# Performance work log

Measured on AMD Instinct MI355X. Metric: run time of the kernel, lower is better.

## Reference

```python
import jax, jax.numpy as jnp
import numpy as np

B, C, H, W = 8, 3, 256, 256
K = 32          # num_kernels
P = 7           # patch_size (hard-coded in CUTSEncoder)
HALF = P // 2
NUM_PATCHES = 32
BN_EPS = 1e-5


def _conv_bn_lrelu(x, w, b, gamma, beta):
    # Conv2d(kernel=3, padding='same') + BatchNorm2d (training-mode batch stats) + leaky_relu(0.01)
    y = jax.lax.conv_general_dilated(x, w, window_strides=(1, 1), padding='SAME',
                                     dimension_numbers=('NCHW', 'OIHW', 'NCHW'))
    y = y + b[None, :, None, None]
    m = jnp.mean(y, axis=(0, 2, 3), keepdims=True)
    v = jnp.var(y, axis=(0, 2, 3), keepdims=True)
    y = (y - m) * jax.lax.rsqrt(v + BN_EPS)
    y = gamma[None, :, None, None] * y + beta[None, :, None, None]
    return jax.nn.leaky_relu(y, negative_slope=0.01)


def setup_inputs() -> dict:
    key = jax.random.key(0)
    ks = jax.random.split(key, 16)
    image = jax.random.normal(ks[0], (B, C, H, W), dtype=jnp.float32)
    # coordinates in [HALF, H - P + HALF] so every centered 7x7 slice is in-bounds
    def xy(k):
        return jax.random.randint(k, (B, NUM_PATCHES, 2), HALF, H - P + HALF + 1, dtype=jnp.int32)
    anchors_xy = xy(ks[1])
    positives_xy = xy(ks[2])
    negatives_xy = xy(ks[3])
    conv1_w = jax.random.normal(ks[4], (K, C, 3, 3), jnp.float32) * 0.1
    conv1_b = jnp.zeros((K,), jnp.float32)
    conv2_w = jax.random.normal(ks[5], (2 * K, K, 3, 3), jnp.float32) * 0.06
    conv2_b = jnp.zeros((2 * K,), jnp.float32)
    conv3_w = jax.random.normal(ks[6], (4 * K, 2 * K, 3, 3), jnp.float32) * 0.04
    conv3_b = jnp.zeros((4 * K,), jnp.float32)
    bn1_g, bn1_b = jnp.ones((K,), jnp.float32), jnp.zeros((K,), jnp.float32)
    bn2_g, bn2_b = jnp.ones((2 * K,), jnp.float32), jnp.zeros((2 * K,), jnp.float32)
    bn3_g, bn3_b = jnp.ones((4 * K,), jnp.float32), jnp.zeros((4 * K,), jnp.float32)
    recon_w = jax.random.normal(ks[7], (C * P * P, 4 * K), jnp.float32) * 0.05
    recon_b = jnp.zeros((C * P * P,), jnp.float32)
    return dict(image=image, anchors_xy=anchors_xy, positives_xy=positives_xy,
                negatives_xy=negatives_xy, conv1_w=conv1_w, conv1_b=conv1_b,
                bn1_g=bn1_g, bn1_b=bn1_b, conv2_w=conv2_w, conv2_b=conv2_b,
                bn2_g=bn2_g, bn2_b=bn2_b, conv3_w=conv3_w, conv3_b=conv3_b,
                bn3_g=bn3_g, bn3_b=bn3_b, recon_w=recon_w, recon_b=recon_b)


def reference(image, anchors_xy, positives_xy, negatives_xy,
              conv1_w, conv1_b, bn1_g, bn1_b,
              conv2_w, conv2_b, bn2_g, bn2_b,
              conv3_w, conv3_b, bn3_g, bn3_b,
              recon_w, recon_b):
    z = _conv_bn_lrelu(image, conv1_w, conv1_b, bn1_g, bn1_b)
    z = _conv_bn_lrelu(z, conv2_w, conv2_b, bn2_g, bn2_b)
    z = _conv_bn_lrelu(z, conv3_w, conv3_b, bn3_g, bn3_b)   # [B, 4K, H, W]

    # In the source, the inner patch loop overwrites the buffers every iteration,
    # so only the LAST patch index survives. Gather exactly that, vectorized over batch.
    a_xy = anchors_xy[:, -1, :]
    p_xy = positives_xy[:, -1, :]
    n_xy = negatives_xy[:, -1, :]

    def slice_patch(img, xy):  # img: [C,H,W], xy: [2]
        return jax.lax.dynamic_slice(img, (0, xy[0] - HALF, xy[1] - HALF), (C, P, P))

    anchor_patches = jax.vmap(slice_patch)(image, a_xy)     # [B, C, P, P]
    positive_patches = jax.vmap(slice_patch)(image, p_xy)
    negative_patches = jax.vmap(slice_patch)(image, n_xy)

    def gather_feat(zb, xy):  # zb: [4K,H,W]
        return jax.lax.dynamic_slice(zb, (0, xy[0], xy[1]), (4 * K, 1, 1)).reshape(4 * K)

    # NOTE: source indexes z at negatives_xy (faithfully replicated)
    encoded_anchor_patches = jax.vmap(gather_feat)(z, n_xy)  # [B, 4K]

    # x_recon is computed in the source but not returned; keep the compute for faithfulness
    _x_recon = encoded_anchor_patches @ recon_w.T + recon_b

    return (anchor_patches, positive_patches, negative_patches, encoded_anchor_patches)
```

## Files before the change

kernel.cpp:

```cpp
#include <hip/hip_runtime.h>
#include <math.h>

#define HH 256
#define WW 256
#define BATCH 8
#define HWSZ 65536
#define NPB2 4096

typedef __attribute__((ext_vector_type(8))) short short8;
typedef __attribute__((ext_vector_type(4))) float floatx4;

__device__ __forceinline__ unsigned short f2bf(float f) {
  union { float f; unsigned int u; } v; v.f = f;
  return (unsigned short)((v.u + 0x8000u) >> 16);
}
__device__ __forceinline__ unsigned int pack2bf(float a, float d) {
  union { float f; unsigned int u; } va, vd; va.f = a; vd.f = d;
  return ((va.u + 0x8000u) >> 16) | ((vd.u + 0x8000u) & 0xffff0000u);
}
__device__ __forceinline__ float bf2f(unsigned short u) {
  union { unsigned int u; float f; } v; v.u = ((unsigned int)u) << 16;
  return v.f;
}

__global__ __launch_bounds__(256) void conv1_mfma(
    const float* __restrict__ img, const float* __restrict__ w1,
    const float* __restrict__ bias, unsigned short* __restrict__ out,
    float* __restrict__ partial,
    const float* __restrict__ w2, const float* __restrict__ w3,
    unsigned short* __restrict__ wf2, unsigned short* __restrict__ wf3)
{
  const int lin = blockIdx.x;
  if (lin >= 4096) {
    int idx = (lin - 4096) * 256 + threadIdx.x;
    if (idx < 18432) {
      const int j = idx & 7;
      const int lane = (idx >> 3) & 63;
      int rest = idx >> 9;
      const int ng = rest % 4;
      const int tap = rest / 4;
      const int cout = ng * 16 + (lane & 15);
      const int cin = ((lane >> 4) << 3) + j;
      wf2[idx] = f2bf(w2[((size_t)cout * 32 + cin) * 9 + tap]);
    } else {
      idx -= 18432;
      if (idx >= 73728) return;
      const int j = idx & 7;
      const int lane = (idx >> 3) & 63;
      int rest = idx >> 9;
      const int ng = rest % 8; rest /= 8;
      const int kc = rest & 1;
      const int tap = rest >> 1;
      const int cout = ng * 16 + (lane & 15);
      const int cin = kc * 32 + ((lane >> 4) << 3) + j;
      wf3[idx] = f2bf(w3[((size_t)cout * 64 + cin) * 9 + tap]);
    }
    return;
  }

  const int tid = threadIdx.x, lane = tid & 63, wv = tid >> 6;
  const int wave_m = wv >> 1, wave_n = wv & 1;
  const int xcd = lin & 7, slot = lin >> 3;
  const int b = slot >> 6;
  const int rem = slot & 63;
  const int h0 = ((xcd << 4) + (rem >> 2)) * 2;
  const int w0 = (rem & 3) * 64;

  __shared__ __align__(16) unsigned short simg[4 * 66 * 4];
  __shared__ __align__(16) unsigned short swf[2 * 64 * 8];
  __shared__ float red2[2][4][16];

  for (int t = tid; t < (4 * 66 * 4) / 2; t += 256)
    ((unsigned int*)simg)[t] = 0u;
  {
    const int t0 = tid * 4;
    #pragma unroll
    for (int u = 0; u < 4; ++u) {
      const int idx = t0 + u;
      const int j = idx & 7, l8 = (idx >> 3) & 63, nt = idx >> 9;
      const int k = ((l8 >> 4) << 3) + j;
      const int cout = nt * 16 + (l8 & 15);
      swf[idx] = (k < 27) ? f2bf(w1[cout * 27 + k]) : (unsigned short)0;
    }
  }
  __syncthreads();
  for (int t = tid; t < 792; t += 256) {
    const int ci = t / 264, r2 = t - ci * 264;
    const int r = r2 / 66, px = r2 - r * 66;
    const int hi = h0 + r - 1, wi = w0 + px - 1;
    if ((unsigned)hi < 256u && (unsigned)wi < 256u)
      simg[(r * 66 + px) * 4 + ci] =
          f2bf(img[((size_t)(b * 3 + ci) * 256 + hi) * 256 + wi]);
  }
  __syncthreads();

  const int j15 = lane & 15, q4 = lane >> 4;
  int off[8];
  #pragma unroll
  for (int j = 0; j < 8; ++j) {
    const int k = q4 * 8 + j;
    const int ci = k / 9, tap = k - ci * 9;
    const int dh = tap / 3, dw = tap - dh * 3;
    off[j] = (dh * 66 + dw) * 4 + ci;
  }
  const int base_px = wave_m * 32 + j15;
  const short8 bg = *(const short8*)&swf[(wave_n * 64 + lane) * 8];

  floatx4 acc[2][2];
  #pragma unroll
  for (int rr = 0; rr < 2; ++rr)
    #pragma unroll
    for (int mf = 0; mf < 2; ++mf) {
      acc[rr][mf] = (floatx4){0.f, 0.f, 0.f, 0.f};
      union { short8 v; unsigned short e[8]; } a;
      const int ab = (rr * 66 + base_px + mf * 16) * 4;
      #pragma unroll
      for (int j = 0; j < 8; ++j) a.e[j] = simg[ab + off[j]];
      acc[rr][mf] = __builtin_amdgcn_mfma_f32_16x16x32_bf16(a.v, bg, acc[rr][mf], 0, 0, 0);
    }

  float sa = 0.f, qa = 0.f;
  const float bv = bias[wave_n * 16 + j15];
  #pragma unroll
  for (int rr = 0; rr < 2; ++rr) {
    const size_t orow = ((size_t)(b * 256 + (h0 + rr)) * 256 + w0);
    #pragma unroll
    for (int mf = 0; mf < 2; ++mf)
      #pragma unroll
      for (int r4 = 0; r4 < 4; ++r4) {
        float y = acc[rr][mf][r4] + bv;
        sa += y; qa += y * y;
        const int p = wave_m * 32 + mf * 16 + q4 * 4 + r4;
        out[(orow + p) * 32 + wave_n * 16 + j15] = f2bf(y);
      }
  }
  sa += __shfl_xor(sa, 16); sa += __shfl_xor(sa, 32);
  qa += __shfl_xor(qa, 16); qa += __shfl_xor(qa, 32);
  if (lane < 16) { red2[0][wv][lane] = sa; red2[1][wv][lane] = qa; }
  __syncthreads();
  if (tid < 64) {
    const int c = tid >> 1, jj = tid & 1;
    const int wn = c >> 4, li = c & 15;
    const float r = red2[jj][wn][li] + red2[jj][wn + 2][li];
    partial[((size_t)c * 2 + jj) * NPB2 + lin] = r;
  }
}

template<int CIN, int COUT, bool WRITE_OUT, int MINW>
__global__ __launch_bounds__(256, MINW) void conv_mfma(
    const unsigned short* __restrict__ in, const unsigned short* __restrict__ wf,
    const float* __restrict__ bias,
    const float* __restrict__ bn_sc, const float* __restrict__ bn_sh,
    unsigned short* __restrict__ out, float* __restrict__ partial)
{
  constexpr int KC = CIN / 32;
  constexpr int NG = COUT / 16;
  constexpr int NF = COUT / 32;
  constexpr int CH8 = CIN / 8;
  constexpr int CH8_LOG = (CH8 == 4) ? 2 : 3;
  constexpr int CPAD = CIN + 8;
  constexpr int CHUNKS = 4 * 66 * CH8;

  const int tid = threadIdx.x, lane = tid & 63, wv = tid >> 6;
  const int wave_m = wv >> 1, wave_n = wv & 1;

  const int lin = blockIdx.x;
  const int xcd = lin & 7, slot = lin >> 3;
  const int b = slot >> 6;
  const int rem = slot & 63;
  const int h0 = ((xcd << 4) + (rem >> 2)) * 2;
  const int w0 = (rem & 3) * 64;
  const size_t inb = (size_t)b * HWSZ * CIN;

  __shared__ __align__(16) unsigned short lds[4 * 66 * CPAD];

  for (int c = tid; c < CHUNKS; c += 256) {
    const int r = c / (66 * CH8);
    const int rem2 = c - r * (66 * CH8);
    const int px = rem2 >> CH8_LOG, ck = rem2 & (CH8 - 1);
    const int hi = h0 + r - 1, wi = w0 - 1 + px;
    uint4 v = make_uint4(0u, 0u, 0u, 0u);
    if ((unsigned)hi < 256u && (unsigned)wi < 256u) {
      uint4 raw = *(const uint4*)&in[inb + ((size_t)hi * 256 + wi) * CIN + ck * 8];
      const float4 s0 = *(const float4*)&bn_sc[ck * 8];
      const float4 s1 = *(const float4*)&bn_sc[ck * 8 + 4];
      const float4 t0 = *(const float4*)&bn_sh[ck * 8];
      const float4 t1 = *(const float4*)&bn_sh[ck * 8 + 4];
      const float scs[8] = {s0.x, s0.y, s0.z, s0.w, s1.x, s1.y, s1.z, s1.w};
      const float shs[8] = {t0.x, t0.y, t0.z, t0.w, t1.x, t1.y, t1.z, t1.w};
      unsigned int* u = (unsigned int*)&raw;
      unsigned int* o = (unsigned int*)&v;
      #pragma unroll
      for (int p = 0; p < 4; ++p) {
        float a = bf2f((unsigned short)(u[p] & 0xffff));
        float d = bf2f((unsigned short)(u[p] >> 16));
        float ya = a * scs[2 * p] + shs[2 * p];
        float yd = d * scs[2 * p + 1] + shs[2 * p + 1];
        ya = fmaxf(ya, 0.01f * ya);
        yd = fmaxf(yd, 0.01f * yd);
        o[p] = pack2bf(ya, yd);
      }
    }
    *(uint4*)&lds[(r * 66 + px) * CPAD + ck * 8] = v;
  }
  __syncthreads();

  const int j15 = lane & 15, q4 = lane >> 4;
  const int base_px = wave_m * 32 + j15;
  const unsigned short* abase = &lds[base_px * CPAD + q4 * 8];

  floatx4 acc[2][2][NF];
  #pragma unroll
  for (int rr = 0; rr < 2; ++rr)
    #pragma unroll
    for (int mf = 0; mf < 2; ++mf)
      #pragma unroll
      for (int nf = 0; nf < NF; ++nf) acc[rr][mf][nf] = (floatx4){0.f, 0.f, 0.f, 0.f};

  #pragma unroll
  for (int dh = 0; dh < 3; ++dh) {
    #pragma unroll
    for (int dw = 0; dw < 3; ++dw) {
      #pragma unroll
      for (int kc = 0; kc < KC; ++kc) {
        const int tap = dh * 3 + dw;
        short8 bg[NF];
        #pragma unroll
        for (int nf = 0; nf < NF; ++nf)
          bg[nf] = *(const short8*)&wf[((((tap * KC + kc) * NG) + wave_n * NF + nf) * 64 + lane) * 8];
        #pragma unroll
        for (int rr = 0; rr < 2; ++rr) {
          short8 a[2];
          #pragma unroll
          for (int mf = 0; mf < 2; ++mf)
            a[mf] = *(const short8*)&abase[((rr + dh) * 66 + dw + mf * 16) * CPAD + kc * 32];
          #pragma unroll
          for (int mf = 0; mf < 2; ++mf)
            #pragma unroll
            for (int nf = 0; nf < NF; ++nf)
              acc[rr][mf][nf] = __builtin_amdgcn_mfma_f32_16x16x32_bf16(a[mf], bg[nf], acc[rr][mf][nf], 0, 0, 0);
        }
      }
    }
  }

  float bv[NF], sa[NF], qa[NF];
  #pragma unroll
  for (int nf = 0; nf < NF; ++nf) {
    bv[nf] = bias[wave_n * (COUT / 2) + nf * 16 + j15];
    sa[nf] = 0.f; qa[nf] = 0.f;
  }
  #pragma unroll
  for (int rr = 0; rr < 2; ++rr) {
    const size_t orow = ((size_t)(b * 256 + (h0 + rr)) * 256 + w0);
    #pragma unroll
    for (int nf = 0; nf < NF; ++nf) {
      const int ch = wave_n * (COUT / 2) + nf * 16 + j15;
      #pragma unroll
      for (int mf = 0; mf < 2; ++mf)
        #pragma unroll
        for (int r4 = 0; r4 < 4; ++r4) {
          float y = acc[rr][mf][nf][r4] + bv[nf];
          sa[nf] += y; qa[nf] += y * y;
          if constexpr (WRITE_OUT) {
            const int p = wave_m * 32 + mf * 16 + q4 * 4 + r4;
            out[(orow + p) * COUT + ch] = f2bf(y);
          }
        }
    }
  }

  __syncthreads();
  float* red = (float*)lds;
  #pragma unroll
  for (int nf = 0; nf < NF; ++nf) {
    float s = sa[nf], q = qa[nf];
    s += __shfl_xor(s, 16); s += __shfl_xor(s, 32);
    q += __shfl_xor(q, 16); q += __shfl_xor(q, 32);
    if (lane < 16) {
      red[(wv * NF + nf) * 16 + lane] = s;
      red[4 * NF * 16 + (wv * NF + nf) * 16 + lane] = q;
    }
  }
  __syncthreads();
  if (tid < COUT) {
    const int wn = tid / (COUT / 2), rr = tid % (COUT / 2);
    const int nf = rr >> 4, li = rr & 15;
    float s = red[(wn * NF + nf) * 16 + li] + red[((wn + 2) * NF + nf) * 16 + li];
    float q = red[4 * NF * 16 + (wn * NF + nf) * 16 + li] +
              red[4 * NF * 16 + ((wn + 2) * NF + nf) * 16 + li];
    partial[((size_t)tid * 2 + 0) * NPB2 + lin] = s;
    partial[((size_t)tid * 2 + 1) * NPB2 + lin] = q;
  }
}

__global__ __launch_bounds__(256) void reduce_stats(
    const float* __restrict__ partial, const float* __restrict__ gamma,
    const float* __restrict__ beta, float* __restrict__ scale,
    float* __restrict__ shift, int npb)
{
  const int c = blockIdx.x;
  float s = 0.f, q = 0.f;
  for (int i = threadIdx.x; i < npb; i += 256) {
    s += partial[((size_t)c * 2 + 0) * npb + i];
    q += partial[((size_t)c * 2 + 1) * npb + i];
  }
  #pragma unroll
  for (int o = 32; o > 0; o >>= 1) { s += __shfl_down(s, o); q += __shfl_down(q, o); }
  __shared__ float rs[4][2];
  const int lane = threadIdx.x & 63, wv = threadIdx.x >> 6;
  if (lane == 0) { rs[wv][0] = s; rs[wv][1] = q; }
  __syncthreads();
  if (threadIdx.x == 0) {
    s = rs[0][0] + rs[1][0] + rs[2][0] + rs[3][0];
    q = rs[0][1] + rs[1][1] + rs[2][1] + rs[3][1];
    const float N = (float)((size_t)BATCH * HWSZ);
    float mean = s / N;
    float var = q / N - mean * mean;
    float rstd = 1.0f / sqrtf(var + 1e-5f);
    float sc = gamma[c] * rstd;
    scale[c] = sc;
    shift[c] = beta[c] - mean * sc;
  }
}

__global__ __launch_bounds__(256) void outputs_kernel(
    const float* __restrict__ img, const int* __restrict__ axy,
    const int* __restrict__ pxy, const int* __restrict__ nxy,
    const unsigned short* __restrict__ y2, const float* __restrict__ wgt,
    const float* __restrict__ bias,
    const float* __restrict__ sc2, const float* __restrict__ sh2,
    const float* __restrict__ scale, const float* __restrict__ shift,
    float* __restrict__ out)
{
  if (blockIdx.x < 14) {
    const int i = blockIdx.x * 256 + threadIdx.x;
    if (i >= 3 * BATCH * 3 * 49) return;
    const int arr = i / 1176, r = i % 1176;
    const int b = r / 147, q = r % 147;
    const int c = q / 49, s = q % 49;
    const int ph = s / 7, pw = s % 7;
    const int* xy = (arr == 0) ? axy : ((arr == 1) ? pxy : nxy);
    const int x = xy[(b * 32 + 31) * 2 + 0];
    const int y = xy[(b * 32 + 31) * 2 + 1];
    out[i] = img[((size_t)(b * 3 + c) * HH + (x - 3 + ph)) * WW + (y - 3 + pw)];
  } else {
    const int b = blockIdx.x - 14;
    const int x = nxy[(b * 32 + 31) * 2 + 0];
    const int y = nxy[(b * 32 + 31) * 2 + 1];
    __shared__ float act[576];
    for (int t = threadIdx.x; t < 576; t += 256) {
      const int ci = t / 9, tap = t - ci * 9;
      const int dh = tap / 3, dw = tap - dh * 3;
      float v = bf2f(y2[((size_t)(b * 256 + (x + dh - 1)) * 256 + (y + dw - 1)) * 64 + ci]);
      v = v * sc2[ci] + sh2[ci];
      act[t] = fmaxf(v, 0.01f * v);
    }
    __syncthreads();
    if (threadIdx.x < 128) {
      const int co = threadIdx.x;
      float acc = bias[co];
      const float4* w4 = (const float4*)(wgt + (size_t)co * 576);
      #pragma unroll 9
      for (int kk = 0; kk < 144; ++kk) {
        const float4 wv = w4[kk];
        acc = fmaf(wv.x, act[4 * kk + 0], acc);
        acc = fmaf(wv.y, act[4 * kk + 1], acc);
        acc = fmaf(wv.z, act[4 * kk + 2], acc);
        acc = fmaf(wv.w, act[4 * kk + 3], acc);
      }
      const float yv = acc * scale[co] + shift[co];
      out[3528 + b * 128 + co] = fmaxf(yv, 0.01f * yv);
    }
  }
}

extern "C" void kernel_launch(void* const* d_in, const int* in_sizes, int n_in,
                              void* d_out, int out_size, void* d_ws, size_t ws_size,
                              hipStream_t stream)
{
  const float* image = (const float*)d_in[0];
  const int* axy = (const int*)d_in[1];
  const int* pxy = (const int*)d_in[2];
  const int* nxy = (const int*)d_in[3];
  const float* c1w = (const float*)d_in[4];
  const float* c1b = (const float*)d_in[5];
  const float* g1 = (const float*)d_in[6];
  const float* b1 = (const float*)d_in[7];
  const float* c2w = (const float*)d_in[8];
  const float* c2b = (const float*)d_in[9];
  const float* g2 = (const float*)d_in[10];
  const float* b2 = (const float*)d_in[11];
  const float* c3w = (const float*)d_in[12];
  const float* c3b = (const float*)d_in[13];
  const float* g3 = (const float*)d_in[14];
  const float* b3 = (const float*)d_in[15];
  float* out = (float*)d_out;

  unsigned short* zb1 = (unsigned short*)d_ws;
  unsigned short* zb2 = zb1 + (size_t)8 * 32 * HWSZ;
  unsigned short* wf2 = zb2 + (size_t)8 * 64 * HWSZ;
  unsigned short* wf3 = wf2 + 18432;
  float* partial = (float*)(wf3 + 73728);
  float* scale1 = partial + (size_t)128 * 2 * NPB2;
  float* shift1 = scale1 + 32;
  float* scale2 = shift1 + 32;
  float* shift2 = scale2 + 64;
  float* scale3 = shift2 + 64;
  float* shift3 = scale3 + 128;

  conv1_mfma<<<4456, 256, 0, stream>>>(
      image, c1w, c1b, zb1, partial, c2w, c3w, wf2, wf3);
  reduce_stats<<<32, 256, 0, stream>>>(partial, g1, b1, scale1, shift1, NPB2);

  conv_mfma<32, 64, true, 2><<<4096, 256, 0, stream>>>(
      zb1, wf2, c2b, scale1, shift1, zb2, partial);
  reduce_stats<<<64, 256, 0, stream>>>(partial, g2, b2, scale2, shift2, NPB2);

  conv_mfma<64, 128, false, 2><<<4096, 256, 0, stream>>>(
      zb2, wf3, c3b, scale2, shift2, nullptr, partial);
  reduce_stats<<<128, 256, 0, stream>>>(partial, g3, b3, scale3, shift3, NPB2);

  outputs_kernel<<<22, 256, 0, stream>>>(image, axy, pxy, nxy, zb2, c3w, c3b,
                                         scale2, shift2, scale3, shift3, out);
}
```

Baseline: 259.1 us.

## Replace per-block BN partials and reduce kernels with slotted atomics folded into consumers

```diff
diff --git a/kernel.cpp b/kernel.cpp
--- a/kernel.cpp
+++ b/kernel.cpp
@@ -5,7 +5,8 @@
 #define WW 256
 #define BATCH 8
 #define HWSZ 65536
-#define NPB2 4096
+#define BN_N 524288.0f
+#define NSLOT 64
 
 typedef __attribute__((ext_vector_type(8))) short short8;
 typedef __attribute__((ext_vector_type(4))) float floatx4;
@@ -26,7 +27,7 @@
 __global__ __launch_bounds__(256) void conv1_mfma(
     const float* __restrict__ img, const float* __restrict__ w1,
     const float* __restrict__ bias, unsigned short* __restrict__ out,
-    float* __restrict__ partial,
+    float* __restrict__ totals1,
     const float* __restrict__ w2, const float* __restrict__ w3,
     unsigned short* __restrict__ wf2, unsigned short* __restrict__ wf3)
 {
@@ -142,7 +143,7 @@
     const int c = tid >> 1, jj = tid & 1;
     const int wn = c >> 4, li = c & 15;
     const float r = red2[jj][wn][li] + red2[jj][wn + 2][li];
-    partial[((size_t)c * 2 + jj) * NPB2 + lin] = r;
+    atomicAdd(&totals1[(((size_t)(lin & (NSLOT - 1)) * 2 + jj)) * 32 + c], r);
   }
 }
 
@@ -150,8 +151,9 @@
 __global__ __launch_bounds__(256, MINW) void conv_mfma(
     const unsigned short* __restrict__ in, const unsigned short* __restrict__ wf,
     const float* __restrict__ bias,
-    const float* __restrict__ bn_sc, const float* __restrict__ bn_sh,
-    unsigned short* __restrict__ out, float* __restrict__ partial)
+    const float* __restrict__ totals_in, const float* __restrict__ gamma_in,
+    const float* __restrict__ beta_in,
+    unsigned short* __restrict__ out, float* __restrict__ totals_out)
 {
   constexpr int KC = CIN / 32;
   constexpr int NG = COUT / 16;
@@ -173,6 +175,23 @@
   const size_t inb = (size_t)b * HWSZ * CIN;
 
   __shared__ __align__(16) unsigned short lds[4 * 66 * CPAD];
+  __shared__ __align__(16) float scsh[2][CIN];
+
+  if (tid < CIN) {
+    float s = 0.f, q = 0.f;
+    #pragma unroll 8
+    for (int i = 0; i < NSLOT; ++i) {
+      s += totals_in[((size_t)i * 2 + 0) * CIN + tid];
+      q += totals_in[((size_t)i * 2 + 1) * CIN + tid];
+    }
+    const float mean = s / BN_N;
+    const float var = q / BN_N - mean * mean;
+    const float rstd = rsqrtf(var + 1e-5f);
+    const float sc = gamma_in[tid] * rstd;
+    scsh[0][tid] = sc;
+    scsh[1][tid] = beta_in[tid] - mean * sc;
+  }
+  __syncthreads();
 
   for (int c = tid; c < CHUNKS; c += 256) {
     const int r = c / (66 * CH8);
@@ -182,10 +201,10 @@
     uint4 v = make_uint4(0u, 0u, 0u, 0u);
     if ((unsigned)hi < 256u && (unsigned)wi < 256u) {
       uint4 raw = *(const uint4*)&in[inb + ((size_t)hi * 256 + wi) * CIN + ck * 8];
-      const float4 s0 = *(const float4*)&bn_sc[ck * 8];
-      const float4 s1 = *(const float4*)&bn_sc[ck * 8 + 4];
-      const float4 t0 = *(const float4*)&bn_sh[ck * 8];
-      const float4 t1 = *(const float4*)&bn_sh[ck * 8 + 4];
+      const float4 s0 = *(const float4*)&scsh[0][ck * 8];
+      const float4 s1 = *(const float4*)&scsh[0][ck * 8 + 4];
+      const float4 t0 = *(const float4*)&scsh[1][ck * 8];
+      const float4 t1 = *(const float4*)&scsh[1][ck * 8 + 4];
       const float scs[8] = {s0.x, s0.y, s0.z, s0.w, s1.x, s1.y, s1.z, s1.w};
       const float shs[8] = {t0.x, t0.y, t0.z, t0.w, t1.x, t1.y, t1.z, t1.w};
       unsigned int* u = (unsigned int*)&raw;
@@ -289,38 +308,9 @@
     float s = red[(wn * NF + nf) * 16 + li] + red[((wn + 2) * NF + nf) * 16 + li];
     float q = red[4 * NF * 16 + (wn * NF + nf) * 16 + li] +
               red[4 * NF * 16 + ((wn + 2) * NF + nf) * 16 + li];
-    partial[((size_t)tid * 2 + 0) * NPB2 + lin] = s;
-    partial[((size_t)tid * 2 + 1) * NPB2 + lin] = q;
-  }
-}
-
-__global__ __launch_bounds__(256) void reduce_stats(
-    const float* __restrict__ partial, const float* __restrict__ gamma,
-    const float* __restrict__ beta, float* __restrict__ scale,
-    float* __restrict__ shift, int npb)
-{
-  const int c = blockIdx.x;
-  float s = 0.f, q = 0.f;
-  for (int i = threadIdx.x; i < npb; i += 256) {
-    s += partial[((size_t)c * 2 + 0) * npb + i];
-    q += partial[((size_t)c * 2 + 1) * npb + i];
-  }
-  #pragma unroll
-  for (int o = 32; o > 0; o >>= 1) { s += __shfl_down(s, o); q += __shfl_down(q, o); }
-  __shared__ float rs[4][2];
-  const int lane = threadIdx.x & 63, wv = threadIdx.x >> 6;
-  if (lane == 0) { rs[wv][0] = s; rs[wv][1] = q; }
-  __syncthreads();
-  if (threadIdx.x == 0) {
-    s = rs[0][0] + rs[1][0] + rs[2][0] + rs[3][0];
-    q = rs[0][1] + rs[1][1] + rs[2][1] + rs[3][1];
-    const float N = (float)((size_t)BATCH * HWSZ);
-    float mean = s / N;
-    float var = q / N - mean * mean;
-    float rstd = 1.0f / sqrtf(var + 1e-5f);
-    float sc = gamma[c] * rstd;
-    scale[c] = sc;
-    shift[c] = beta[c] - mean * sc;
+    const int sl = lin & (NSLOT - 1);
+    atomicAdd(&totals_out[((size_t)sl * 2 + 0) * COUT + tid], s);
+    atomicAdd(&totals_out[((size_t)sl * 2 + 1) * COUT + tid], q);
   }
 }
 
@@ -329,8 +319,10 @@
     const int* __restrict__ pxy, const int* __restrict__ nxy,
     const unsigned short* __restrict__ y2, const float* __restrict__ wgt,
     const float* __restrict__ bias,
-    const float* __restrict__ sc2, const float* __restrict__ sh2,
-    const float* __restrict__ scale, const float* __restrict__ shift,
+    const float* __restrict__ totals2, const float* __restrict__ g2,
+    const float* __restrict__ b2v,
+    const float* __restrict__ totals3, const float* __restrict__ g3,
+    const float* __restrict__ b3v,
     float* __restrict__ out)
 {
   if (blockIdx.x < 14) {
@@ -348,12 +340,40 @@
     const int b = blockIdx.x - 14;
     const int x = nxy[(b * 32 + 31) * 2 + 0];
     const int y = nxy[(b * 32 + 31) * 2 + 1];
+    __shared__ float sc2[2][64], sc3[2][128];
     __shared__ float act[576];
+    if (threadIdx.x < 64) {
+      float s = 0.f, q = 0.f;
+      for (int i = 0; i < NSLOT; ++i) {
+        s += totals2[((size_t)i * 2 + 0) * 64 + threadIdx.x];
+        q += totals2[((size_t)i * 2 + 1) * 64 + threadIdx.x];
+      }
+      const float mean = s / BN_N;
+      const float var = q / BN_N - mean * mean;
+      const float rstd = rsqrtf(var + 1e-5f);
+      const float sc = g2[threadIdx.x] * rstd;
+      sc2[0][threadIdx.x] = sc;
+      sc2[1][threadIdx.x] = b2v[threadIdx.x] - mean * sc;
+    } else if (threadIdx.x >= 128) {
+      const int c = threadIdx.x - 128;
+      float s = 0.f, q = 0.f;
+      for (int i = 0; i < NSLOT; ++i) {
+        s += totals3[((size_t)i * 2 + 0) * 128 + c];
+        q += totals3[((size_t)i * 2 + 1) * 128 + c];
+      }
+      const float mean = s / BN_N;
+      const float var = q / BN_N - mean * mean;
+      const float rstd = rsqrtf(var + 1e-5f);
+      const float sc = g3[c] * rstd;
+      sc3[0][c] = sc;
+      sc3[1][c] = b3v[c] - mean * sc;
+    }
+    __syncthreads();
     for (int t = threadIdx.x; t < 576; t += 256) {
       const int ci = t / 9, tap = t - ci * 9;
       const int dh = tap / 3, dw = tap - dh * 3;
       float v = bf2f(y2[((size_t)(b * 256 + (x + dh - 1)) * 256 + (y + dw - 1)) * 64 + ci]);
-      v = v * sc2[ci] + sh2[ci];
+      v = v * sc2[0][ci] + sc2[1][ci];
       act[t] = fmaxf(v, 0.01f * v);
     }
     __syncthreads();
@@ -369,7 +389,7 @@
         acc = fmaf(wv.z, act[4 * kk + 2], acc);
         acc = fmaf(wv.w, act[4 * kk + 3], acc);
       }
-      const float yv = acc * scale[co] + shift[co];
+      const float yv = acc * sc3[0][co] + sc3[1][co];
       out[3528 + b * 128 + co] = fmaxf(yv, 0.01f * yv);
     }
   }
@@ -401,26 +421,22 @@
   unsigned short* zb2 = zb1 + (size_t)8 * 32 * HWSZ;
   unsigned short* wf2 = zb2 + (size_t)8 * 64 * HWSZ;
   unsigned short* wf3 = wf2 + 18432;
-  float* partial = (float*)(wf3 + 73728);
-  float* scale1 = partial + (size_t)128 * 2 * NPB2;
-  float* shift1 = scale1 + 32;
-  float* scale2 = shift1 + 32;
-  float* shift2 = scale2 + 64;
-  float* scale3 = shift2 + 64;
-  float* shift3 = scale3 + 128;
+  float* totals1 = (float*)(wf3 + 73728);
+  float* totals2 = totals1 + (size_t)NSLOT * 2 * 32;
+  float* totals3 = totals2 + (size_t)NSLOT * 2 * 64;
+
+  hipMemsetAsync(totals1, 0, (size_t)NSLOT * 2 * (32 + 64 + 128) * sizeof(float),
+                 stream);
 
   conv1_mfma<<<4456, 256, 0, stream>>>(
-      image, c1w, c1b, zb1, partial, c2w, c3w, wf2, wf3);
-  reduce_stats<<<32, 256, 0, stream>>>(partial, g1, b1, scale1, shift1, NPB2);
+      image, c1w, c1b, zb1, totals1, c2w, c3w, wf2, wf3);
 
   conv_mfma<32, 64, true, 2><<<4096, 256, 0, stream>>>(
-      zb1, wf2, c2b, scale1, shift1, zb2, partial);
-  reduce_stats<<<64, 256, 0, stream>>>(partial, g2, b2, scale2, shift2, NPB2);
+      zb1, wf2, c2b, totals1, g1, b1, zb2, totals2);
 
   conv_mfma<64, 128, false, 2><<<4096, 256, 0, stream>>>(
-      zb2, wf3, c3b, scale2, shift2, nullptr, partial);
-  reduce_stats<<<128, 256, 0, stream>>>(partial, g3, b3, scale3, shift3, NPB2);
+      zb2, wf3, c3b, totals2, g2, b2, nullptr, totals3);
 
   outputs_kernel<<<22, 256, 0, stream>>>(image, axy, pxy, nxy, zb2, c3w, c3b,
-                                         scale2, shift2, scale3, shift3, out);
-}
+                                         totals2, g2, b2, totals3, g3, b3, out);
+}
```

After: 248.2 us. -4.2%, faster.
